# Performance work log

Hardware: AMD Instinct MI355X
Metric: run time of the kernel (lower is better)

Reference implementation:

```python
import jax, jax.numpy as jnp
import numpy as np

WS = 7          # window size (square)
SHIFT = 3       # shift size
NH = 8          # num heads
DIM = 256
B, H, W = 32, 56, 56


def _relative_position_index(ws: int) -> np.ndarray:
    coords = np.stack(np.meshgrid(np.arange(ws), np.arange(ws), indexing='ij'))  # (2, ws, ws)
    cf = coords.reshape(2, -1)                                                   # (2, N)
    rel = cf[:, :, None] - cf[:, None, :]                                        # (2, N, N)
    rel = rel.transpose(1, 2, 0).copy()
    rel[:, :, 0] += ws - 1
    rel[:, :, 1] += ws - 1
    rel[:, :, 0] *= 2 * ws - 1
    return rel.sum(-1).reshape(-1).astype(np.int32)                              # (N*N,)


def _shift_mask(h: int, w: int, ws: int, shift: int) -> np.ndarray:
    img = np.zeros((h, w), dtype=np.float32)
    cnt = 0
    for hs in ((0, -ws), (-ws, -shift), (-shift, None)):
        for wsl in ((0, -ws), (-ws, -shift), (-shift, None)):
            img[hs[0]:hs[1], wsl[0]:wsl[1]] = cnt
            cnt += 1
    nwh, nww = h // ws, w // ws
    m = img.reshape(nwh, ws, nww, ws).transpose(0, 2, 1, 3).reshape(nwh * nww, ws * ws)
    am = m[:, None, :] - m[:, :, None]                 # (nW, N, N)
    return np.where(am != 0, np.float32(-100.0), np.float32(0.0))


def setup_inputs() -> dict:
    key = jax.random.key(0)
    ks = jax.random.split(key, 5)
    x = jax.random.normal(ks[0], (B, H, W, DIM), jnp.float32)
    qkv_weight = jax.random.normal(ks[1], (3 * DIM, DIM), jnp.float32) * 0.02
    qkv_bias = jnp.zeros((3 * DIM,), jnp.float32)
    proj_weight = jax.random.normal(ks[2], (DIM, DIM), jnp.float32) * 0.02
    proj_bias = jnp.zeros((DIM,), jnp.float32)
    rel_bias_table = jax.random.normal(ks[3], ((2 * WS - 1) ** 2, NH), jnp.float32) * 0.02
    rel_pos_index = jnp.asarray(_relative_position_index(WS))
    return {
        'x': x, 'qkv_weight': qkv_weight, 'qkv_bias': qkv_bias,
        'proj_weight': proj_weight, 'proj_bias': proj_bias,
        'rel_bias_table': rel_bias_table, 'rel_pos_index': rel_pos_index,
    }


def reference(x, qkv_weight, qkv_bias, proj_weight, proj_bias, rel_bias_table, rel_pos_index):
    b, h, w, c = x.shape
    n = WS * WS
    hd = c // NH
    nwh, nww = h // WS, w // WS
    nw = nwh * nww

    # relative position bias: (1, NH, N, N)
    bias = rel_bias_table[rel_pos_index].reshape(n, n, NH).transpose(2, 0, 1)[None]

    # cyclic shift
    xs = jnp.roll(x, (-SHIFT, -SHIFT), axis=(1, 2))

    # window partition -> (B*nW, N, C)
    xw = xs.reshape(b, nwh, WS, nww, WS, c).transpose(0, 1, 3, 2, 4, 5).reshape(b * nw, n, c)

    qkv = xw @ qkv_weight.T + qkv_bias
    qkv = qkv.reshape(b * nw, n, 3, NH, hd).transpose(2, 0, 3, 1, 4)  # (3, B*nW, NH, N, hd)
    q = qkv[0] * (hd ** -0.5)
    k = qkv[1]
    v = qkv[2]

    attn = jnp.einsum('bhnd,bhmd->bhnm', q, k) + bias                # (B*nW, NH, N, N)

    # shift mask (static)
    amask = jnp.asarray(_shift_mask(h, w, WS, SHIFT))                # (nW, N, N)
    attn = attn.reshape(b, nw, NH, n, n) + amask[None, :, None]
    attn = jax.nn.softmax(attn.reshape(b * nw, NH, n, n), axis=-1)

    out = jnp.einsum('bhnm,bhmd->bhnd', attn, v)                     # (B*nW, NH, N, hd)
    out = out.transpose(0, 2, 1, 3).reshape(b * nw, n, c)
    out = out @ proj_weight.T + proj_bias

    # window reverse + reverse shift
    out = out.reshape(b, nwh, nww, WS, WS, c).transpose(0, 1, 3, 2, 4, 5).reshape(b, h, w, c)
    out = jnp.roll(out, (SHIFT, SHIFT), axis=(1, 2))
    return out
```

## Files before the change

kernel.cpp:

```cpp
#include <hip/hip_runtime.h>
#include <hip/hip_bf16.h>


#define NTOK 49
#define DIM_ 256
#define NH_  8
#define NQKV 196608
#define NPRJ 65536
#define NTAB1 19208
#define NTAB4 (4 * NTAB1)

#define WSP_B  393216ull
#define TAB_B  524288ull
#define Q_B    831744ull
#define Q_BYTES 51380224ull
#define K_B    (Q_B + Q_BYTES)
#define VT_B   (K_B + Q_BYTES)
#define VT_BYTES 58720256ull
#define NEED_BIG (VT_B + VT_BYTES)
#define NEED_TAB (TAB_B + (unsigned long long)NTAB4 * 4)

typedef short v8s __attribute__((ext_vector_type(8)));
typedef float v4f __attribute__((ext_vector_type(4)));
typedef float v16f __attribute__((ext_vector_type(16)));

#define MFMA16 __builtin_amdgcn_mfma_f32_16x16x32_bf16
#define MFMA32 __builtin_amdgcn_mfma_f32_32x32x16_bf16
#define LGKM_WAIT() asm volatile("s_waitcnt lgkmcnt(0)" ::: "memory")

static __device__ __forceinline__ v8s zero_v8s() {
    v8s z = {0, 0, 0, 0, 0, 0, 0, 0};
    return z;
}

static __device__ __forceinline__ v16f zero_v16f() {
    v16f z;
    #pragma unroll
    for (int i = 0; i < 16; ++i) z[i] = 0.0f;
    return z;
}

static __device__ __forceinline__ v8s lds_frag(const __hip_bfloat16* p, int row,
                                               int stride, int koff, int nrows) {
    if (row < nrows) return *(const v8s*)(p + row * stride + koff);
    return zero_v8s();
}

static __device__ __forceinline__ v8s cvt8(const float* p) {
    v4f a = *(const v4f*)p;
    v4f b = *(const v4f*)(p + 4);
    union { v8s v; __hip_bfloat16 h[8]; } r;
    r.h[0] = __float2bfloat16(a[0]); r.h[1] = __float2bfloat16(a[1]);
    r.h[2] = __float2bfloat16(a[2]); r.h[3] = __float2bfloat16(a[3]);
    r.h[4] = __float2bfloat16(b[0]); r.h[5] = __float2bfloat16(b[1]);
    r.h[6] = __float2bfloat16(b[2]); r.h[7] = __float2bfloat16(b[3]);
    return r.v;
}

__global__ __launch_bounds__(256) void prep_kernel(
    const float* __restrict__ qkvW, const float* __restrict__ projW,
    const float* __restrict__ rbt, const int* __restrict__ rpi,
    __hip_bfloat16* __restrict__ wsQ, __hip_bfloat16* __restrict__ wsP,
    float* __restrict__ tab4, int doTab)
{
    int i = blockIdx.x * 256 + threadIdx.x;
    if (i < NQKV) { wsQ[i] = __float2bfloat16(qkvW[i]); return; }
    int j = i - NQKV;
    if (j < NPRJ) { wsP[j] = __float2bfloat16(projW[j]); return; }
    int t = j - NPRJ;
    if (!doTab || t >= NTAB4) return;
    int cls = t / NTAB1, rem = t - cls * NTAB1;
    int h = rem / 2401, p = rem - h * 2401;
    int row = p / 49, col = p - row * 49;
    int rh = (cls & 1) ? (((row / 7) < 4) ? 1 : 2) : 0;
    int rw = (cls & 2) ? (((row % 7) < 4) ? 1 : 2) : 0;
    int ch = (cls & 1) ? (((col / 7) < 4) ? 1 : 2) : 0;
    int cw = (cls & 2) ? (((col % 7) < 4) ? 1 : 2) : 0;
    float mask = ((rh * 3 + rw) != (ch * 3 + cw)) ? -100.0f : 0.0f;
    tab4[t] = rbt[rpi[p] * NH_ + h] + mask;
}

__global__ __launch_bounds__(256) void qkvattn_kernel(
    const float* __restrict__ x,
    const float* __restrict__ qkvB,
    const __hip_bfloat16* __restrict__ wsQ,
    const float* __restrict__ tab4,
    __hip_bfloat16* __restrict__ OH)
{
    constexpr int SXS = 264;
    constexpr int QKS = 40;
    constexpr int VTS = 72;
    constexpr int PS  = 72;
    constexpr int WVSZ = 2 * NTOK * QKS + 32 * VTS;

    __shared__ alignas(16) __hip_bfloat16 s_x[NTOK * SXS];
    __shared__ alignas(16) __hip_bfloat16 s_wv[4 * WVSZ];

    const int tid = threadIdx.x, wave = tid >> 6, lane = tid & 63;
    const int quad = lane >> 4, l16 = lane & 15;
    const int l32 = lane & 31, half = lane >> 5;
    const int win = blockIdx.x;
    const int b = win >> 6, wh = (win >> 3) & 7, wwi = win & 7;
    const int cls = ((wh == 7) ? 1 : 0) | ((wwi == 7) ? 2 : 0);

    __hip_bfloat16* wq  = s_wv + wave * WVSZ;
    __hip_bfloat16* wk  = wq + NTOK * QKS;
    __hip_bfloat16* wvt = wq + 2 * NTOK * QKS;
    __hip_bfloat16* wp  = wq;

    for (int i = lane; i < 32 * 7; i += 64)
        wvt[(i / 7) * VTS + 49 + (i % 7)] = __float2bfloat16(0.0f);

    for (int i = tid; i < NTOK * 64; i += 256) {
        int tok = i >> 6, f4 = (i & 63) * 4;
        int r = tok / 7, c = tok - r * 7;
        int hg = wh * 7 + r + 3; if (hg >= 56) hg -= 56;
        int wg = wwi * 7 + c + 3; if (wg >= 56) wg -= 56;
        float4 v = *(const float4*)(x + ((b * 56 + hg) * 56 + wg) * DIM_ + f4);
        __hip_bfloat16* dst = s_x + tok * SXS + f4;
        dst[0] = __float2bfloat16(v.x);
        dst[1] = __float2bfloat16(v.y);
        dst[2] = __float2bfloat16(v.z);
        dst[3] = __float2bfloat16(v.w);
    }
    __syncthreads();

    const float qscale = 0.17677669529663687f;
    const int r1 = (32 + l32 < NTOK) ? (32 + l32) : 0;
    const __hip_bfloat16* arow0 = s_x + l32 * SXS + half * 8;
    const __hip_bfloat16* arow1 = s_x + r1 * SXS + half * 8;

    for (int hp = 0; hp < 2; ++hp) {
        const int h = wave * 2 + hp;

        #pragma unroll
        for (int m = 0; m < 3; ++m) {
            const int nb = m * 256 + h * 32;
            const __hip_bfloat16* wrow = wsQ + (nb + l32) * DIM_ + half * 8;
            v16f acc0 = zero_v16f(), acc1 = zero_v16f();

            if (m < 2) {
                #pragma unroll
                for (int kh = 0; kh < 2; ++kh) {
                    v8s wf[8];
                    #pragma unroll
                    for (int k = 0; k < 8; ++k)
                        wf[k] = *(const v8s*)(wrow + kh * 128 + k * 16);
                    #pragma unroll
                    for (int k = 0; k < 8; ++k) {
                        v8s a0 = *(const v8s*)(arow0 + kh * 128 + k * 16);
                        v8s a1 = *(const v8s*)(arow1 + kh * 128 + k * 16);
                        acc0 = MFMA32(a0, wf[k], acc0, 0, 0, 0);
                        acc1 = MFMA32(a1, wf[k], acc1, 0, 0, 0);
                    }
                }
                float bias = qkvB[nb + l32];
                float sc = (m == 0) ? qscale : 1.0f;
                __hip_bfloat16* dst = (m == 0) ? wq : wk;
                #pragma unroll
                for (int rg = 0; rg < 16; ++rg) {
                    int rowoff = (rg & 3) + 8 * (rg >> 2) + 4 * half;
                    dst[rowoff * QKS + l32] =
                        __float2bfloat16((acc0[rg] + bias) * sc);
                    int tok1 = 32 + rowoff;
                    if (tok1 < NTOK)
                        dst[tok1 * QKS + l32] =
                            __float2bfloat16((acc1[rg] + bias) * sc);
                }
            } else {
                #pragma unroll
                for (int kh = 0; kh < 2; ++kh) {
                    v8s wf[8];
                    #pragma unroll
                    for (int k = 0; k < 8; ++k)
                        wf[k] = *(const v8s*)(wrow + kh * 128 + k * 16);
                    #pragma unroll
                    for (int k = 0; k < 8; ++k) {
                        v8s b0 = *(const v8s*)(arow0 + kh * 128 + k * 16);
                        v8s b1 = *(const v8s*)(arow1 + kh * 128 + k * 16);
                        acc0 = MFMA32(wf[k], b0, acc0, 0, 0, 0);
                        acc1 = MFMA32(wf[k], b1, acc1, 0, 0, 0);
                    }
                }
                const int tok1 = 32 + l32;
                #pragma unroll
                for (int rg = 0; rg < 16; ++rg) {
                    int feat = (rg & 3) + 8 * (rg >> 2) + 4 * half;
                    float bias = qkvB[nb + feat];
                    wvt[feat * VTS + l32] = __float2bfloat16(acc0[rg] + bias);
                    if (tok1 < NTOK)
                        wvt[feat * VTS + tok1] = __float2bfloat16(acc1[rg] + bias);
                }
            }
        }
        LGKM_WAIT();

        const float* tabh = tab4 + (cls * NH_ + h) * 2401;
        __hip_bfloat16* qs = OH + (win * NH_ + h) * (NTOK * 32);

        v8s qa[4], kb[4];
        #pragma unroll
        for (int mt = 0; mt < 4; ++mt) {
            qa[mt] = lds_frag(wq, mt * 16 + l16, QKS, quad * 8, NTOK);
            kb[mt] = lds_frag(wk, mt * 16 + l16, QKS, quad * 8, NTOK);
        }
        v8s pb[2][2];
        #pragma unroll
        for (int nt = 0; nt < 2; ++nt) {
            const __hip_bfloat16* vr = wvt + (nt * 16 + l16) * VTS;
            pb[nt][0] = *(const v8s*)(vr + quad * 8);
            pb[nt][1] = (quad == 3) ? zero_v8s() : *(const v8s*)(vr + 32 + quad * 8);
        }
        LGKM_WAIT();

        #pragma unroll
        for (int mtile = 0; mtile < 4; ++mtile) {
            v4f sa[4];
            #pragma unroll
            for (int nt = 0; nt < 4; ++nt) {
                v4f z = {0.f, 0.f, 0.f, 0.f};
                sa[nt] = MFMA16(qa[mtile], kb[nt], z, 0, 0, 0);
            }
            #pragma unroll
            for (int rg = 0; rg < 4; ++rg) {
                int row = mtile * 16 + quad * 4 + rg;
                bool rok = row < NTOK;
                float v[4];
                float rmax = -1e30f;
                #pragma unroll
                for (int nt = 0; nt < 4; ++nt) {
                    int col = nt * 16 + l16;
                    float s = -1e30f;
                    if (rok && col < NTOK)
                        s = sa[nt][rg] + tabh[row * 49 + col];
                    v[nt] = s;
                    rmax = fmaxf(rmax, s);
                }
                #pragma unroll
                for (int mm = 8; mm >= 1; mm >>= 1)
                    rmax = fmaxf(rmax, __shfl_xor(rmax, mm, 64));
                float rsum = 0.f;
                #pragma unroll
                for (int nt = 0; nt < 4; ++nt) {
                    float e = (v[nt] <= -1e29f) ? 0.f : __expf(v[nt] - rmax);
                    v[nt] = e;
                    rsum += e;
                }
                #pragma unroll
                for (int mm = 8; mm >= 1; mm >>= 1)
                    rsum += __shfl_xor(rsum, mm, 64);
                if (rok) {
                    float inv = 1.0f / rsum;
                    #pragma unroll
                    for (int nt = 0; nt < 4; ++nt)
                        wp[row * PS + nt * 16 + l16] = __float2bfloat16(v[nt] * inv);
                }
            }
        }
        LGKM_WAIT();

        #pragma unroll
        for (int mtile = 0; mtile < 4; ++mtile) {
            v8s pa0 = lds_frag(wp, mtile * 16 + l16, PS, quad * 8, NTOK);
            v8s pa1 = lds_frag(wp, mtile * 16 + l16, PS, 32 + quad * 8, NTOK);
            #pragma unroll
            for (int nt = 0; nt < 2; ++nt) {
                v4f z = {0.f, 0.f, 0.f, 0.f};
                v4f acc = MFMA16(pa0, pb[nt][0], z, 0, 0, 0);
                acc = MFMA16(pa1, pb[nt][1], acc, 0, 0, 0);
                #pragma unroll
                for (int rg = 0; rg < 4; ++rg) {
                    int tok = mtile * 16 + quad * 4 + rg;
                    if (tok < NTOK)
                        qs[tok * 32 + nt * 16 + l16] = __float2bfloat16(acc[rg]);
                }
            }
        }
        LGKM_WAIT();
    }
}

__global__ __launch_bounds__(256) void proj_kernel(
    const __hip_bfloat16* __restrict__ OH,
    const __hip_bfloat16* __restrict__ wsP,
    const float* __restrict__ projB,
    float* __restrict__ out)
{
    const int tid = threadIdx.x, wave = tid >> 6, lane = tid & 63;
    const int quad = lane >> 4, l16 = lane & 15;
    const int win = blockIdx.x;
    const int b = win >> 6, wh = (win >> 3) & 7, wwi = win & 7;
    const int m0 = wave * 16;

    const __hip_bfloat16* ohw = OH + (size_t)win * (NH_ * NTOK * 32);
    v8s af[8];
    int tokA = m0 + l16;
    #pragma unroll
    for (int ks = 0; ks < 8; ++ks)
        af[ks] = (tokA < NTOK)
                   ? *(const v8s*)(ohw + ks * (NTOK * 32) + tokA * 32 + quad * 8)
                   : zero_v8s();

    int ooff[4];
    #pragma unroll
    for (int rg = 0; rg < 4; ++rg) {
        int row = m0 + quad * 4 + rg;
        if (row < NTOK) {
            int r = row / 7, c = row - r * 7;
            int hg = wh * 7 + r + 3; if (hg >= 56) hg -= 56;
            int wg = wwi * 7 + c + 3; if (wg >= 56) wg -= 56;
            ooff[rg] = ((b * 56 + hg) * 56 + wg) * DIM_;
        } else ooff[rg] = -1;
    }

    #pragma unroll
    for (int t = 0; t < 16; ++t) {
        const __hip_bfloat16* wrow = wsP + (t * 16 + l16) * DIM_;
        v4f acc = {0.f, 0.f, 0.f, 0.f};
        #pragma unroll
        for (int ks = 0; ks < 8; ++ks) {
            v8s bfr = *(const v8s*)(wrow + ks * 32 + quad * 8);
            acc = MFMA16(af[ks], bfr, acc, 0, 0, 0);
        }
        float pbv = projB[t * 16 + l16];
        #pragma unroll
        for (int rg = 0; rg < 4; ++rg)
            if (ooff[rg] >= 0)
                out[ooff[rg] + t * 16 + l16] = acc[rg] + pbv;
    }
}

__global__ __launch_bounds__(256, 2) void swin_attn_fused(
    const float* __restrict__ x,
    const float* __restrict__ qkvB,
    const float* __restrict__ projB,
    const float* __restrict__ rbt,
    const int*   __restrict__ rpi,
    const __hip_bfloat16* __restrict__ wsQ,
    const __hip_bfloat16* __restrict__ wsP,
    const float* __restrict__ biasTab,
    float*       __restrict__ out)
{
    constexpr int QKS = 40;
    constexpr int VTS = 72;
    constexpr int PS  = 72;
    constexpr int OS  = 264;
    constexpr int WVSZ = 6224;

    __shared__ alignas(16) __hip_bfloat16 s_wv[4 * WVSZ];
    __shared__ alignas(16) __hip_bfloat16 s_o[NTOK * OS];
    __shared__ int s_off[NTOK];
    __shared__ int s_reg[NTOK];

    const int tid  = threadIdx.x;
    const int wave = tid >> 6;
    const int lane = tid & 63;
    const int quad = lane >> 4;
    const int l16  = lane & 15;

    const int wid  = blockIdx.x;
    const int b    = wid >> 6;
    const int wIdx = wid & 63;
    const int wh   = wIdx >> 3;
    const int wwi  = wIdx & 7;

    if (tid < NTOK) {
        int r = tid / 7, c = tid - r * 7;
        int hs = wh * 7 + r, ws = wwi * 7 + c;
        int hg = hs + 3; if (hg >= 56) hg -= 56;
        int wg = ws + 3; if (wg >= 56) wg -= 56;
        s_off[tid] = ((b * 56 + hg) * 56 + wg) * DIM_;
        int rh = (hs < 49) ? 0 : ((hs < 53) ? 1 : 2);
        int rw = (ws < 49) ? 0 : ((ws < 53) ? 1 : 2);
        s_reg[tid] = rh * 3 + rw;
    }

    __hip_bfloat16* wq  = s_wv + wave * WVSZ;
    __hip_bfloat16* wk  = wq + NTOK * QKS;
    __hip_bfloat16* wvt = wq + 2 * NTOK * QKS;
    __hip_bfloat16* wp  = wq;

    for (int i = lane; i < 32 * 15; i += 64) {
        int f = i / 15, kk = 49 + (i % 15);
        wvt[f * VTS + kk] = __float2bfloat16(0.0f);
    }
    __syncthreads();

    const float qscale = 0.17677669529663687f;

    for (int hp = 0; hp < 2; ++hp) {
        const int h = wave * 2 + hp;
        LGKM_WAIT();

        for (int mh = 0; mh < 2; ++mh) {
            const int mbase = mh * 32;
            v8s at[2][8];
            #pragma unroll
            for (int sub = 0; sub < 2; ++sub) {
                int tok = mbase + sub * 16 + l16;
                const float* xr = (tok < NTOK) ? (x + s_off[tok]) : nullptr;
                #pragma unroll
                for (int ks = 0; ks < 8; ++ks)
                    at[sub][ks] = xr ? cvt8(xr + ks * 32 + quad * 8) : zero_v8s();
            }
            #pragma unroll
            for (int t = 0; t < 6; ++t) {
                int mat = t >> 1, ntile = t & 1;
                int nout = mat * 256 + h * 32 + ntile * 16 + l16;
                const __hip_bfloat16* wrow = wsQ + nout * DIM_;
                v4f a0 = {0.f, 0.f, 0.f, 0.f}, a1 = {0.f, 0.f, 0.f, 0.f};
                #pragma unroll
                for (int ks = 0; ks < 8; ++ks) {
                    v8s bfr = *(const v8s*)(wrow + ks * 32 + quad * 8);
                    a0 = MFMA16(at[0][ks], bfr, a0, 0, 0, 0);
                    a1 = MFMA16(at[1][ks], bfr, a1, 0, 0, 0);
                }
                float bias  = qkvB[nout];
                float scale = (mat == 0) ? qscale : 1.0f;
                #pragma unroll
                for (int sub = 0; sub < 2; ++sub) {
                    v4f acc = sub ? a1 : a0;
                    #pragma unroll
                    for (int rg = 0; rg < 4; ++rg) {
                        int row = mbase + sub * 16 + quad * 4 + rg;
                        if (row < NTOK) {
                            float val = (acc[rg] + bias) * scale;
                            int col = ntile * 16 + l16;
                            __hip_bfloat16 bv = __float2bfloat16(val);
                            if (mat == 0)      wq[row * QKS + col] = bv;
                            else if (mat == 1) wk[row * QKS + col] = bv;
                            else               wvt[col * VTS + row] = bv;
                        }
                    }
                }
            }
        }
        LGKM_WAIT();

        v8s qa[4], kb[4];
        #pragma unroll
        for (int i = 0; i < 4; ++i) {
            qa[i] = lds_frag(wq, i * 16 + l16, QKS, quad * 8, NTOK);
            kb[i] = lds_frag(wk, i * 16 + l16, QKS, quad * 8, NTOK);
        }
        int regc[4];
        #pragma unroll
        for (int nt = 0; nt < 4; ++nt) {
            int col = nt * 16 + l16;
            regc[nt] = (col < NTOK) ? s_reg[col] : -1;
        }
        LGKM_WAIT();
        const float* tabh = biasTab ? (biasTab + h * 2401) : nullptr;
        #pragma unroll
        for (int mtile = 0; mtile < 4; ++mtile) {
            v4f sa[4];
            #pragma unroll
            for (int nt = 0; nt < 4; ++nt) {
                v4f z = {0.f, 0.f, 0.f, 0.f};
                sa[nt] = MFMA16(qa[mtile], kb[nt], z, 0, 0, 0);
            }
            #pragma unroll
            for (int rg = 0; rg < 4; ++rg) {
                int row = mtile * 16 + quad * 4 + rg;
                bool rok = row < NTOK;
                int rr = rok ? s_reg[row] : -2;
                float v[4];
                float rmax = -1e30f;
                #pragma unroll
                for (int nt = 0; nt < 4; ++nt) {
                    int col = nt * 16 + l16;
                    float s = -1e30f;
                    if (rok && col < NTOK) {
                        float bv = tabh ? tabh[row * 49 + col]
                                        : rbt[rpi[row * 49 + col] * NH_ + h];
                        s = sa[nt][rg] + bv;
                        if (rr != regc[nt]) s -= 100.0f;
                    }
                    v[nt] = s;
                    rmax = fmaxf(rmax, s);
                }
                #pragma unroll
                for (int mm = 8; mm >= 1; mm >>= 1)
                    rmax = fmaxf(rmax, __shfl_xor(rmax, mm, 64));
                float rsum = 0.f;
                #pragma unroll
                for (int nt = 0; nt < 4; ++nt) {
                    float e = (v[nt] <= -1e29f) ? 0.f : __expf(v[nt] - rmax);
                    v[nt] = e;
                    rsum += e;
                }
                #pragma unroll
                for (int mm = 8; mm >= 1; mm >>= 1)
                    rsum += __shfl_xor(rsum, mm, 64);
                if (rok) {
                    float inv = 1.0f / rsum;
                    #pragma unroll
                    for (int nt = 0; nt < 4; ++nt)
                        wp[row * PS + nt * 16 + l16] = __float2bfloat16(v[nt] * inv);
                }
            }
        }
        LGKM_WAIT();

        v8s pb[2][2];
        #pragma unroll
        for (int nt = 0; nt < 2; ++nt)
            #pragma unroll
            for (int ks = 0; ks < 2; ++ks)
                pb[nt][ks] = *(const v8s*)(wvt + (nt * 16 + l16) * VTS + ks * 32 + quad * 8);
        #pragma unroll
        for (int mtile = 0; mtile < 4; ++mtile) {
            v8s pa0 = lds_frag(wp, mtile * 16 + l16, PS, quad * 8, NTOK);
            v8s pa1 = lds_frag(wp, mtile * 16 + l16, PS, 32 + quad * 8, NTOK);
            #pragma unroll
            for (int nt = 0; nt < 2; ++nt) {
                v4f z = {0.f, 0.f, 0.f, 0.f};
                v4f acc = MFMA16(pa0, pb[nt][0], z, 0, 0, 0);
                acc = MFMA16(pa1, pb[nt][1], acc, 0, 0, 0);
                #pragma unroll
                for (int rg = 0; rg < 4; ++rg) {
                    int row = mtile * 16 + quad * 4 + rg;
                    if (row < NTOK)
                        s_o[row * OS + h * 32 + nt * 16 + l16] = __float2bfloat16(acc[rg]);
                }
            }
        }
    }
    __syncthreads();

    {
        int m0 = wave * 16;
        v8s af[8];
        #pragma unroll
        for (int ks = 0; ks < 8; ++ks)
            af[ks] = lds_frag(s_o, m0 + l16, OS, ks * 32 + quad * 8, NTOK);
        #pragma unroll
        for (int t = 0; t < 16; ++t) {
            const __hip_bfloat16* wrow = wsP + (t * 16 + l16) * DIM_;
            v4f acc = {0.f, 0.f, 0.f, 0.f};
            #pragma unroll
            for (int ks = 0; ks < 8; ++ks) {
                v8s bfr = *(const v8s*)(wrow + ks * 32 + quad * 8);
                acc = MFMA16(af[ks], bfr, acc, 0, 0, 0);
            }
            float pbv = projB[t * 16 + l16];
            #pragma unroll
            for (int rg = 0; rg < 4; ++rg) {
                int row = m0 + quad * 4 + rg;
                if (row < NTOK)
                    out[s_off[row] + t * 16 + l16] = acc[rg] + pbv;
            }
        }
    }
}

extern "C" void kernel_launch(void* const* d_in, const int* in_sizes, int n_in,
                              void* d_out, int out_size, void* d_ws, size_t ws_size,
                              hipStream_t stream) {
    const float* x     = (const float*)d_in[0];
    const float* qkvW  = (const float*)d_in[1];
    const float* qkvB  = (const float*)d_in[2];
    const float* projW = (const float*)d_in[3];
    const float* projB = (const float*)d_in[4];
    const float* rbt   = (const float*)d_in[5];
    const int*   rpi   = (const int*)d_in[6];
    float* o = (float*)d_out;

    __hip_bfloat16* wsQ = (__hip_bfloat16*)d_ws;
    __hip_bfloat16* wsP = (__hip_bfloat16*)((char*)d_ws + WSP_B);
    float* tab4         = (float*)((char*)d_ws + TAB_B);
    __hip_bfloat16* OH  = (__hip_bfloat16*)((char*)d_ws + Q_B);

    const int prepBlocks = (NQKV + NPRJ + NTAB4 + 255) / 256;

    if (ws_size >= NEED_BIG) {
        prep_kernel<<<prepBlocks, 256, 0, stream>>>(qkvW, projW, rbt, rpi,
                                                    wsQ, wsP, tab4, 1);
        qkvattn_kernel<<<2048, 256, 0, stream>>>(x, qkvB, wsQ, tab4, OH);
        proj_kernel<<<2048, 256, 0, stream>>>(OH, wsP, projB, o);
    } else {
        int doTab = (ws_size >= NEED_TAB) ? 1 : 0;
        prep_kernel<<<prepBlocks, 256, 0, stream>>>(qkvW, projW, rbt, rpi,
                                                    wsQ, wsP, tab4, doTab);
        swin_attn_fused<<<2048, 256, 0, stream>>>(x, qkvB, projB, rbt, rpi,
                                                  wsQ, wsP, doTab ? tab4 : nullptr, o);
    }
}
```

Baseline: 486.6 us.

## Pad bias/mask table to 64x64, transpose softmax MFMA, regroup proj blocks

The combined bias-plus-mask table is padded to a 64x64 layout per class and head, with -1e30 in the padded entries. This lets the attention kernel load it as aligned float4 vectors with no bounds checks. The score MFMA is transposed (K x Q) so that each lane holds 16 values of one query row. The row reductions then take two cross-lane shuffles instead of four, and probabilities are written as packed 8-byte stores. The projection kernel now assigns each block 4 windows by 4 output tiles, reusing the loaded weight fragments across windows in exchange for reloading activations per tile.

New measurement: 475.5 us. 1.02x faster.

```diff
diff --git a/kernel.cpp b/kernel.cpp
--- a/kernel.cpp
+++ b/kernel.cpp
@@ -7,18 +7,13 @@
 #define NH_  8
 #define NQKV 196608
 #define NPRJ 65536
-#define NTAB1 19208
-#define NTAB4 (4 * NTAB1)
+#define NTABP 131072
 
 #define WSP_B  393216ull
 #define TAB_B  524288ull
-#define Q_B    831744ull
-#define Q_BYTES 51380224ull
-#define K_B    (Q_B + Q_BYTES)
-#define VT_B   (K_B + Q_BYTES)
-#define VT_BYTES 58720256ull
-#define NEED_BIG (VT_B + VT_BYTES)
-#define NEED_TAB (TAB_B + (unsigned long long)NTAB4 * 4)
+#define Q_B    1048576ull
+#define NEED_BIG 162312448ull
+#define NEED_TAB (TAB_B + (unsigned long long)NTABP * 4)
 
 typedef short v8s __attribute__((ext_vector_type(8)));
 typedef float v4f __attribute__((ext_vector_type(4)));
@@ -61,30 +56,36 @@
     const float* __restrict__ qkvW, const float* __restrict__ projW,
     const float* __restrict__ rbt, const int* __restrict__ rpi,
     __hip_bfloat16* __restrict__ wsQ, __hip_bfloat16* __restrict__ wsP,
-    float* __restrict__ tab4, int doTab)
+    float* __restrict__ tabP, int doTab)
 {
     int i = blockIdx.x * 256 + threadIdx.x;
     if (i < NQKV) { wsQ[i] = __float2bfloat16(qkvW[i]); return; }
     int j = i - NQKV;
     if (j < NPRJ) { wsP[j] = __float2bfloat16(projW[j]); return; }
     int t = j - NPRJ;
-    if (!doTab || t >= NTAB4) return;
-    int cls = t / NTAB1, rem = t - cls * NTAB1;
-    int h = rem / 2401, p = rem - h * 2401;
-    int row = p / 49, col = p - row * 49;
-    int rh = (cls & 1) ? (((row / 7) < 4) ? 1 : 2) : 0;
-    int rw = (cls & 2) ? (((row % 7) < 4) ? 1 : 2) : 0;
-    int ch = (cls & 1) ? (((col / 7) < 4) ? 1 : 2) : 0;
-    int cw = (cls & 2) ? (((col % 7) < 4) ? 1 : 2) : 0;
-    float mask = ((rh * 3 + rw) != (ch * 3 + cw)) ? -100.0f : 0.0f;
-    tab4[t] = rbt[rpi[p] * NH_ + h] + mask;
+    if (!doTab || t >= NTABP) return;
+    int cls = t >> 15;
+    int rem = t & 32767;
+    int h = rem >> 12;
+    int p = rem & 4095;
+    int row = p >> 6, col = p & 63;
+    float val = -1e30f;
+    if (row < NTOK && col < NTOK) {
+        int rh = (cls & 1) ? (((row / 7) < 4) ? 1 : 2) : 0;
+        int rw = (cls & 2) ? (((row % 7) < 4) ? 1 : 2) : 0;
+        int ch = (cls & 1) ? (((col / 7) < 4) ? 1 : 2) : 0;
+        int cw = (cls & 2) ? (((col % 7) < 4) ? 1 : 2) : 0;
+        float mask = ((rh * 3 + rw) != (ch * 3 + cw)) ? -100.0f : 0.0f;
+        val = rbt[rpi[row * 49 + col] * NH_ + h] + mask;
+    }
+    tabP[t] = val;
 }
 
 __global__ __launch_bounds__(256) void qkvattn_kernel(
     const float* __restrict__ x,
     const float* __restrict__ qkvB,
     const __hip_bfloat16* __restrict__ wsQ,
-    const float* __restrict__ tab4,
+    const float* __restrict__ tabP,
     __hip_bfloat16* __restrict__ OH)
 {
     constexpr int SXS = 264;
@@ -195,7 +196,7 @@
         }
         LGKM_WAIT();
 
-        const float* tabh = tab4 + (cls * NH_ + h) * 2401;
+        const float* tabh = tabP + (cls * NH_ + h) * 4096;
         __hip_bfloat16* qs = OH + (win * NH_ + h) * (NTOK * 32);
 
         v8s qa[4], kb[4];
@@ -214,46 +215,48 @@
         LGKM_WAIT();
 
         #pragma unroll
-        for (int mtile = 0; mtile < 4; ++mtile) {
-            v4f sa[4];
-            #pragma unroll
-            for (int nt = 0; nt < 4; ++nt) {
+        for (int ntq = 0; ntq < 4; ++ntq) {
+            const int qtok = ntq * 16 + l16;
+            v4f tv[4];
+            #pragma unroll
+            for (int mt = 0; mt < 4; ++mt)
+                tv[mt] = *(const v4f*)(tabh + qtok * 64 + mt * 16 + quad * 4);
+            v4f st[4];
+            #pragma unroll
+            for (int mt = 0; mt < 4; ++mt) {
                 v4f z = {0.f, 0.f, 0.f, 0.f};
-                sa[nt] = MFMA16(qa[mtile], kb[nt], z, 0, 0, 0);
-            }
-            #pragma unroll
-            for (int rg = 0; rg < 4; ++rg) {
-                int row = mtile * 16 + quad * 4 + rg;
-                bool rok = row < NTOK;
-                float v[4];
-                float rmax = -1e30f;
-                #pragma unroll
-                for (int nt = 0; nt < 4; ++nt) {
-                    int col = nt * 16 + l16;
-                    float s = -1e30f;
-                    if (rok && col < NTOK)
-                        s = sa[nt][rg] + tabh[row * 49 + col];
-                    v[nt] = s;
+                st[mt] = MFMA16(kb[mt], qa[ntq], z, 0, 0, 0);
+            }
+            float v[16];
+            float rmax = -1e30f;
+            #pragma unroll
+            for (int mt = 0; mt < 4; ++mt)
+                #pragma unroll
+                for (int rg = 0; rg < 4; ++rg) {
+                    float s = st[mt][rg] + tv[mt][rg];
+                    v[mt * 4 + rg] = s;
                     rmax = fmaxf(rmax, s);
                 }
-                #pragma unroll
-                for (int mm = 8; mm >= 1; mm >>= 1)
-                    rmax = fmaxf(rmax, __shfl_xor(rmax, mm, 64));
-                float rsum = 0.f;
-                #pragma unroll
-                for (int nt = 0; nt < 4; ++nt) {
-                    float e = (v[nt] <= -1e29f) ? 0.f : __expf(v[nt] - rmax);
-                    v[nt] = e;
-                    rsum += e;
-                }
-                #pragma unroll
-                for (int mm = 8; mm >= 1; mm >>= 1)
-                    rsum += __shfl_xor(rsum, mm, 64);
-                if (rok) {
-                    float inv = 1.0f / rsum;
+            rmax = fmaxf(rmax, __shfl_xor(rmax, 16, 64));
+            rmax = fmaxf(rmax, __shfl_xor(rmax, 32, 64));
+            float rsum = 0.f;
+            #pragma unroll
+            for (int i = 0; i < 16; ++i) {
+                float e = (v[i] <= -1e29f) ? 0.f : __expf(v[i] - rmax);
+                v[i] = e;
+                rsum += e;
+            }
+            rsum += __shfl_xor(rsum, 16, 64);
+            rsum += __shfl_xor(rsum, 32, 64);
+            if (qtok < NTOK) {
+                float inv = 1.0f / rsum;
+                #pragma unroll
+                for (int mt = 0; mt < 4; ++mt) {
+                    union { __hip_bfloat16 h4[4]; unsigned long long u; } pk;
                     #pragma unroll
-                    for (int nt = 0; nt < 4; ++nt)
-                        wp[row * PS + nt * 16 + l16] = __float2bfloat16(v[nt] * inv);
+                    for (int rg = 0; rg < 4; ++rg)
+                        pk.h4[rg] = __float2bfloat16(v[mt * 4 + rg] * inv);
+                    *(unsigned long long*)(wp + qtok * PS + mt * 16 + quad * 4) = pk.u;
                 }
             }
         }
@@ -288,45 +291,55 @@
 {
     const int tid = threadIdx.x, wave = tid >> 6, lane = tid & 63;
     const int quad = lane >> 4, l16 = lane & 15;
-    const int win = blockIdx.x;
-    const int b = win >> 6, wh = (win >> 3) & 7, wwi = win & 7;
+    const int bid = blockIdx.x;
+    const int wg = bid >> 2, tq = bid & 3;
     const int m0 = wave * 16;
-
-    const __hip_bfloat16* ohw = OH + (size_t)win * (NH_ * NTOK * 32);
-    v8s af[8];
-    int tokA = m0 + l16;
+    const int tokA = m0 + l16;
+
+    int ooff[4][4];
     #pragma unroll
-    for (int ks = 0; ks < 8; ++ks)
-        af[ks] = (tokA < NTOK)
-                   ? *(const v8s*)(ohw + ks * (NTOK * 32) + tokA * 32 + quad * 8)
-                   : zero_v8s();
-
-    int ooff[4];
+    for (int wl = 0; wl < 4; ++wl) {
+        int win = wg * 4 + wl;
+        int b = win >> 6, wh = (win >> 3) & 7, wwi = win & 7;
+        #pragma unroll
+        for (int rg = 0; rg < 4; ++rg) {
+            int row = m0 + quad * 4 + rg;
+            if (row < NTOK) {
+                int r = row / 7, c = row - r * 7;
+                int hg = wh * 7 + r + 3; if (hg >= 56) hg -= 56;
+                int wgl = wwi * 7 + c + 3; if (wgl >= 56) wgl -= 56;
+                ooff[wl][rg] = ((b * 56 + hg) * 56 + wgl) * DIM_;
+            } else ooff[wl][rg] = -1;
+        }
+    }
+
     #pragma unroll
-    for (int rg = 0; rg < 4; ++rg) {
-        int row = m0 + quad * 4 + rg;
-        if (row < NTOK) {
-            int r = row / 7, c = row - r * 7;
-            int hg = wh * 7 + r + 3; if (hg >= 56) hg -= 56;
-            int wg = wwi * 7 + c + 3; if (wg >= 56) wg -= 56;
-            ooff[rg] = ((b * 56 + hg) * 56 + wg) * DIM_;
-        } else ooff[rg] = -1;
-    }
-
-    #pragma unroll
-    for (int t = 0; t < 16; ++t) {
+    for (int tt = 0; tt < 4; ++tt) {
+        const int t = tq * 4 + tt;
         const __hip_bfloat16* wrow = wsP + (t * 16 + l16) * DIM_;
-        v4f acc = {0.f, 0.f, 0.f, 0.f};
-        #pragma unroll
-        for (int ks = 0; ks < 8; ++ks) {
-            v8s bfr = *(const v8s*)(wrow + ks * 32 + quad * 8);
-            acc = MFMA16(af[ks], bfr, acc, 0, 0, 0);
-        }
+        v8s wf[8];
+        #pragma unroll
+        for (int ks = 0; ks < 8; ++ks)
+            wf[ks] = *(const v8s*)(wrow + ks * 32 + quad * 8);
         float pbv = projB[t * 16 + l16];
-        #pragma unroll
-        for (int rg = 0; rg < 4; ++rg)
-            if (ooff[rg] >= 0)
-                out[ooff[rg] + t * 16 + l16] = acc[rg] + pbv;
+
+        #pragma unroll
+        for (int wl = 0; wl < 4; ++wl) {
+            const __hip_bfloat16* ohw =
+                OH + (size_t)(wg * 4 + wl) * (NH_ * NTOK * 32);
+            v4f acc = {0.f, 0.f, 0.f, 0.f};
+            #pragma unroll
+            for (int ks = 0; ks < 8; ++ks) {
+                v8s af = (tokA < NTOK)
+                    ? *(const v8s*)(ohw + ks * (NTOK * 32) + tokA * 32 + quad * 8)
+                    : zero_v8s();
+                acc = MFMA16(af, wf[ks], acc, 0, 0, 0);
+            }
+            #pragma unroll
+            for (int rg = 0; rg < 4; ++rg)
+                if (ooff[wl][rg] >= 0)
+                    out[ooff[wl][rg] + t * 16 + l16] = acc[rg] + pbv;
+        }
     }
 }
 
@@ -450,7 +463,7 @@
             regc[nt] = (col < NTOK) ? s_reg[col] : -1;
         }
         LGKM_WAIT();
-        const float* tabh = biasTab ? (biasTab + h * 2401) : nullptr;
+        const float* tabh = biasTab ? (biasTab + h * 4096) : nullptr;
         #pragma unroll
         for (int mtile = 0; mtile < 4; ++mtile) {
             v4f sa[4];
@@ -471,7 +484,7 @@
                     int col = nt * 16 + l16;
                     float s = -1e30f;
                     if (rok && col < NTOK) {
-                        float bv = tabh ? tabh[row * 49 + col]
+                        float bv = tabh ? tabh[row * 64 + col]
                                         : rbt[rpi[row * 49 + col] * NH_ + h];
                         s = sa[nt][rg] + bv;
                         if (rr != regc[nt]) s -= 100.0f;
@@ -568,21 +581,21 @@
 
     __hip_bfloat16* wsQ = (__hip_bfloat16*)d_ws;
     __hip_bfloat16* wsP = (__hip_bfloat16*)((char*)d_ws + WSP_B);
-    float* tab4         = (float*)((char*)d_ws + TAB_B);
+    float* tabP         = (float*)((char*)d_ws + TAB_B);
     __hip_bfloat16* OH  = (__hip_bfloat16*)((char*)d_ws + Q_B);
 
-    const int prepBlocks = (NQKV + NPRJ + NTAB4 + 255) / 256;
+    const int prepBlocks = (NQKV + NPRJ + NTABP + 255) / 256;
 
     if (ws_size >= NEED_BIG) {
         prep_kernel<<<prepBlocks, 256, 0, stream>>>(qkvW, projW, rbt, rpi,
-                                                    wsQ, wsP, tab4, 1);
-        qkvattn_kernel<<<2048, 256, 0, stream>>>(x, qkvB, wsQ, tab4, OH);
+                                                    wsQ, wsP, tabP, 1);
+        qkvattn_kernel<<<2048, 256, 0, stream>>>(x, qkvB, wsQ, tabP, OH);
         proj_kernel<<<2048, 256, 0, stream>>>(OH, wsP, projB, o);
     } else {
         int doTab = (ws_size >= NEED_TAB) ? 1 : 0;
         prep_kernel<<<prepBlocks, 256, 0, stream>>>(qkvW, projW, rbt, rpi,
-                                                    wsQ, wsP, tab4, doTab);
+                                                    wsQ, wsP, tabP, doTab);
         swin_attn_fused<<<2048, 256, 0, stream>>>(x, qkvB, projB, rbt, rpi,
-                                                  wsQ, wsP, doTab ? tab4 : nullptr, o);
-    }
-}
+                                                  wsQ, wsP, doTab ? tabP : nullptr, o);
+    }
+}
```
